# Kernel tuning notes

Hardware: AMD Instinct MI355X
Metric: run time of the kernel (lower is better)

The kernel has to match this reference:

```python
import jax, jax.numpy as jnp
import numpy as np
from jax import lax

SIG_DEPTH = 2
BN_EPS = 1e-5


def zhang_sig(x, depth):
    """Zhang 2D signature of an image batch.

    x: (B, C, H, W). Level-1 term is the total double increment per channel;
    level-(k+1) is built recursively: S_{k+1}[.., c] (i,j) = strict-2D-prefix-sum
    of S_k at (i,j) times the double increment D[c](i,j). Each level k yields
    C^k features (sum over the spatial grid).
    """
    # double (mixed) increments: (B, C, H-1, W-1)
    D = x[:, :, 1:, 1:] - x[:, :, 1:, :-1] - x[:, :, :-1, 1:] + x[:, :, :-1, :-1]
    B, C, h, w = D.shape
    S = D
    levels = [S.sum((-2, -1))]  # (B, C)
    for _ in range(depth - 1):
        # strict 2D prefix sum: P[i,j] = sum_{i'<i, j'<j} S[i',j']
        P = jnp.cumsum(jnp.cumsum(S, axis=-2), axis=-1)
        P = jnp.pad(P, ((0, 0), (0, 0), (1, 0), (1, 0)))[:, :, :-1, :-1]
        # tensor-product with a fresh increment channel: (B, C_prev*C, h, w)
        S = (P[:, :, None] * D[:, None, :]).reshape(B, -1, h, w)
        levels.append(S.sum((-2, -1)))
    return jnp.concatenate(levels, axis=1)  # (B, sum_k C^k)


def setup_inputs() -> dict:
    key = jax.random.key(0)
    ks = jax.random.split(key, 4)
    N, C_IN, C_SIG, HW, NUM_CLASSES = 2048, 64, 32, 8, 100
    F = C_SIG + C_SIG * C_SIG  # 1056 signature features (depth 2)
    feats = jax.random.normal(ks[0], (N, C_IN, HW, HW), dtype=jnp.float32)
    conv_w = jax.random.normal(ks[1], (C_SIG, C_IN, 3, 3), dtype=jnp.float32) * (1.0 / np.sqrt(C_IN * 9))
    bn_gamma = jnp.ones((F,), dtype=jnp.float32)
    bn_beta = jnp.zeros((F,), dtype=jnp.float32)
    lin_w = jax.random.normal(ks[2], (F, F), dtype=jnp.float32) * (1.0 / np.sqrt(F))
    lin_b = jnp.zeros((F,), dtype=jnp.float32)
    fc_w = jax.random.normal(ks[3], (NUM_CLASSES, F), dtype=jnp.float32) * (1.0 / np.sqrt(F))
    fc_b = jnp.zeros((NUM_CLASSES,), dtype=jnp.float32)
    return {"feats": feats, "conv_w": conv_w, "bn_gamma": bn_gamma, "bn_beta": bn_beta,
            "lin_w": lin_w, "lin_b": lin_b, "fc_w": fc_w, "fc_b": fc_b}


def reference(feats, conv_w, bn_gamma, bn_beta, lin_w, lin_b, fc_w, fc_b):
    # Conv2d(64->32, 3x3, stride 1, pad 1, no bias)
    y = lax.conv_general_dilated(
        feats, conv_w, window_strides=(1, 1), padding=((1, 1), (1, 1)),
        dimension_numbers=("NCHW", "OIHW", "NCHW"))
    # Zhang 2D signature pooling -> (N, 1056)
    sig = zhang_sig(y, SIG_DEPTH)
    # BatchNorm1d (training mode: batch statistics, biased variance)
    mean = sig.mean(axis=0)
    var = sig.var(axis=0)
    xn = (sig - mean) * lax.rsqrt(var + BN_EPS)
    h = xn * bn_gamma + bn_beta
    # Linear(F -> F) then classifier Linear(F -> num_classes)
    h = h @ lin_w.T + lin_b
    out = h @ fc_w.T + fc_b
    return out
```

## Files before the change

### kernel.cpp

```cpp
#include <hip/hip_runtime.h>

#define N_B   2048
#define F_SIG 1056
#define F_PAD 1088
#define K_CLS 100
#define K_PAD 128
#define KW_PAD 112
#define DROW   52
#define OSPLIT  8
#define OCHUNK 132
#define XW     72
#define SY     32
#define WF_BLKS 280
#define BF0_BLKS 128

typedef __attribute__((ext_vector_type(8))) short s8v;
typedef __attribute__((ext_vector_type(4))) float f4v;

__device__ __host__ __forceinline__ void split_bf16(float x, unsigned& h, unsigned& l) {
    unsigned u = __builtin_bit_cast(unsigned, x);
    unsigned hb = (u + 0x7FFFu + ((u >> 16) & 1u)) >> 16;
    float hf = __builtin_bit_cast(float, hb << 16);
    float r = x - hf;
    unsigned ur = __builtin_bit_cast(unsigned, r);
    unsigned lb = (ur + 0x7FFFu + ((ur >> 16) & 1u)) >> 16;
    h = hb & 0xFFFFu; l = lb & 0xFFFFu;
}

__global__ void k_wt(const float* __restrict__ cw, unsigned short* __restrict__ Ahi,
                     unsigned short* __restrict__ Alo) {
    int t = blockIdx.x * 256 + threadIdx.x;
    if (t >= 36 * 512) return;
    int f = t >> 9, r = t & 511, lane = r >> 3, e = r & 7;
    int mt = f & 1, ch = (f >> 1) & 1, tap = f >> 2;
    int oc  = mt * 16 + (lane & 15);
    int cin = ch * 32 + (lane >> 4) * 8 + e;
    float v = cw[oc * 576 + cin * 9 + tap];
    unsigned h, l;
    split_bf16(v, h, l);
    Ahi[t] = (unsigned short)h;
    Alo[t] = (unsigned short)l;
}

#define WF_FMA16(sv, vv) do { \
    A0.x = fmaf((sv).x, (vv).x, A0.x); A0.y = fmaf((sv).x, (vv).y, A0.y); \
    A0.z = fmaf((sv).x, (vv).z, A0.z); A0.w = fmaf((sv).x, (vv).w, A0.w); \
    A1.x = fmaf((sv).y, (vv).x, A1.x); A1.y = fmaf((sv).y, (vv).y, A1.y); \
    A1.z = fmaf((sv).y, (vv).z, A1.z); A1.w = fmaf((sv).y, (vv).w, A1.w); \
    A2.x = fmaf((sv).z, (vv).x, A2.x); A2.y = fmaf((sv).z, (vv).y, A2.y); \
    A2.z = fmaf((sv).z, (vv).z, A2.z); A2.w = fmaf((sv).z, (vv).w, A2.w); \
    A3.x = fmaf((sv).w, (vv).x, A3.x); A3.y = fmaf((sv).w, (vv).y, A3.y); \
    A3.z = fmaf((sv).w, (vv).z, A3.z); A3.w = fmaf((sv).w, (vv).w, A3.w); } while (0)

__launch_bounds__(256, 5)
__global__ void k_fused(const float* __restrict__ x,
                        const unsigned short* __restrict__ Ahi,
                        const unsigned short* __restrict__ Alo,
                        float* __restrict__ sig,
                        const float* __restrict__ fcw, const float* __restrict__ lw,
                        float* __restrict__ part,
                        const float* __restrict__ linb, const float* __restrict__ fcb,
                        float* __restrict__ bfv) {
    __shared__ __align__(16) unsigned short xpl[2][100 * XW];
    unsigned short* xhi = xpl[0];
    unsigned short* xlo = xpl[1];
    const int tid = threadIdx.x;
    const int bid = blockIdx.x;

    if (bid < WF_BLKS) {
        const int ibx = bid % 5, ky = (bid / 5) % 7, z = bid / 35;
        const int wv = tid >> 6;
        const int k0 = ky * 16 + wv * 4;
        const int ib = ibx * 256 + (tid & 63) * 4;
        if (ib >= F_SIG) return;
        const float* f0 = fcw + (size_t)min(k0,     K_CLS - 1) * F_SIG;
        const float* f1 = fcw + (size_t)min(k0 + 1, K_CLS - 1) * F_SIG;
        const float* f2 = fcw + (size_t)min(k0 + 2, K_CLS - 1) * F_SIG;
        const float* f3 = fcw + (size_t)min(k0 + 3, K_CLS - 1) * F_SIG;
        const int o0 = z * OCHUNK;
        float4 A0 = {0.f,0.f,0.f,0.f}, A1 = {0.f,0.f,0.f,0.f};
        float4 A2 = {0.f,0.f,0.f,0.f}, A3 = {0.f,0.f,0.f,0.f};
        const float* lwb = lw + (size_t)o0 * F_SIG + ib;
        for (int g = 0; g < OCHUNK / 4; ++g) {
            const int o = o0 + g * 4;
            float4 s0 = *reinterpret_cast<const float4*>(f0 + o);
            float4 s1 = *reinterpret_cast<const float4*>(f1 + o);
            float4 s2 = *reinterpret_cast<const float4*>(f2 + o);
            float4 s3 = *reinterpret_cast<const float4*>(f3 + o);
            const float* lp = lwb + (size_t)(g * 4) * F_SIG;
            float4 v0 = *reinterpret_cast<const float4*>(lp);
            float4 v1 = *reinterpret_cast<const float4*>(lp + F_SIG);
            float4 v2 = *reinterpret_cast<const float4*>(lp + 2 * F_SIG);
            float4 v3 = *reinterpret_cast<const float4*>(lp + 3 * F_SIG);
            float4 sj0 = make_float4(s0.x, s1.x, s2.x, s3.x);
            float4 sj1 = make_float4(s0.y, s1.y, s2.y, s3.y);
            float4 sj2 = make_float4(s0.z, s1.z, s2.z, s3.z);
            float4 sj3 = make_float4(s0.w, s1.w, s2.w, s3.w);
            WF_FMA16(sj0, v0);
            WF_FMA16(sj1, v1);
            WF_FMA16(sj2, v2);
            WF_FMA16(sj3, v3);
        }
        *reinterpret_cast<float4*>(part + ((size_t)z * KW_PAD + k0 + 0) * F_SIG + ib) = A0;
        *reinterpret_cast<float4*>(part + ((size_t)z * KW_PAD + k0 + 1) * F_SIG + ib) = A1;
        *reinterpret_cast<float4*>(part + ((size_t)z * KW_PAD + k0 + 2) * F_SIG + ib) = A2;
        *reinterpret_cast<float4*>(part + ((size_t)z * KW_PAD + k0 + 3) * F_SIG + ib) = A3;
        return;
    }
    if (bid < WF_BLKS + BF0_BLKS) {
        const int k = bid - WF_BLKS;
        float s = 0.f;
        if (k < K_CLS) {
            const float* fr = fcw + (size_t)k * F_SIG;
            for (int o = tid; o < F_SIG; o += 256) s = fmaf(fr[o], linb[o], s);
        }
#pragma unroll
        for (int d = 32; d; d >>= 1) s += __shfl_xor(s, d);
        float* redf = (float*)xhi;
        if ((tid & 63) == 0) redf[tid >> 6] = s;
        __syncthreads();
        if (tid == 0) {
            float tot = redf[0] + redf[1] + redf[2] + redf[3];
            bfv[k] = (k < K_CLS) ? (tot + fcb[k]) : 0.f;
        }
        return;
    }

    const int b = bid - (WF_BLKS + BF0_BLKS);
    float* ysT  = (float*)xpl;
    float* Ds   = ysT + 2304;
    float* Cs   = Ds + 1664;
    float* colS = Cs + 1664;

    for (int e = tid; e < 1296; e += 256) {
        int bb = e / 36, w = e - bb * 36;
        int pp = (bb < 10) ? bb
               : (bb < 20) ? 90 + (bb - 10)
               : ((bb - 20) >> 1) * 10 + 10 + (((bb - 20) & 1) ? 9 : 0);
        reinterpret_cast<unsigned*>(xhi + pp * XW)[w] = 0u;
        reinterpret_cast<unsigned*>(xlo + pp * XW)[w] = 0u;
    }
    const float4* xb4 = reinterpret_cast<const float4*>(x + (size_t)b * 4096);
    {
        float4 v0 = xb4[tid], v1 = xb4[tid + 256], v2 = xb4[tid + 512], v3 = xb4[tid + 768];
#pragma unroll
        for (int u = 0; u < 4; ++u) {
            float4 v = (u == 0) ? v0 : (u == 1) ? v1 : (u == 2) ? v2 : v3;
            int e = tid + u * 256;
            int cin = e >> 4, p = (e & 15) * 4;
            int ih = p >> 3, iw = p & 7;
            int pp = (ih + 1) * 10 + (iw + 1);
            unsigned h, l;
            split_bf16(v.x, h, l); xhi[(pp+0)*XW + cin] = (unsigned short)h; xlo[(pp+0)*XW + cin] = (unsigned short)l;
            split_bf16(v.y, h, l); xhi[(pp+1)*XW + cin] = (unsigned short)h; xlo[(pp+1)*XW + cin] = (unsigned short)l;
            split_bf16(v.z, h, l); xhi[(pp+2)*XW + cin] = (unsigned short)h; xlo[(pp+2)*XW + cin] = (unsigned short)l;
            split_bf16(v.w, h, l); xhi[(pp+3)*XW + cin] = (unsigned short)h; xlo[(pp+3)*XW + cin] = (unsigned short)l;
        }
    }
    __syncthreads();

    f4v accA = {0.f, 0.f, 0.f, 0.f};
    f4v accB = {0.f, 0.f, 0.f, 0.f};
    int pa_, pb_, mt_, kg_;
    {
        const int wv = tid >> 6;
        const int lane = tid & 63;
        const int j16 = lane & 15, kg = lane >> 4;
        const int mt = wv & 1, pt = wv >> 1;
        const int pa = pt * 32 + j16;
        const int pb = pt * 32 + 16 + j16;
        pa_ = pa; pb_ = pb; mt_ = mt; kg_ = kg;
        const int oha = pa >> 3, owa = pa & 7;
        const int ohb = pb >> 3, owb = pb & 7;
        const unsigned short* HbA = xhi + (oha * 10 + owa) * XW + kg * 8;
        const unsigned short* LbA = xlo + (oha * 10 + owa) * XW + kg * 8;
        const unsigned short* HbB = xhi + (ohb * 10 + owb) * XW + kg * 8;
        const unsigned short* LbB = xlo + (ohb * 10 + owb) * XW + kg * 8;
        const uint4* AH = reinterpret_cast<const uint4*>(Ahi) + (size_t)mt * 64 + lane;
        const uint4* AL = reinterpret_cast<const uint4*>(Alo) + (size_t)mt * 64 + lane;
#pragma unroll
        for (int k = 0; k < 18; ++k) {
            const int tap = k >> 1, ch = k & 1;
            const int th = tap / 3, tw = tap % 3;
            const int xoff = (th * 10 + tw) * XW + ch * 32;
            uint4 ah = AH[(size_t)(2 * k) * 64];
            uint4 al = AL[(size_t)(2 * k) * 64];
            uint4 bha = *reinterpret_cast<const uint4*>(HbA + xoff);
            uint4 bla = *reinterpret_cast<const uint4*>(LbA + xoff);
            uint4 bhb = *reinterpret_cast<const uint4*>(HbB + xoff);
            uint4 blb = *reinterpret_cast<const uint4*>(LbB + xoff);
            s8v Ah = __builtin_bit_cast(s8v, ah);
            s8v Al = __builtin_bit_cast(s8v, al);
            s8v BhA = __builtin_bit_cast(s8v, bha);
            s8v BlA = __builtin_bit_cast(s8v, bla);
            s8v BhB = __builtin_bit_cast(s8v, bhb);
            s8v BlB = __builtin_bit_cast(s8v, blb);
            accA = __builtin_amdgcn_mfma_f32_16x16x32_bf16(Ah, BhA, accA, 0, 0, 0);
            accA = __builtin_amdgcn_mfma_f32_16x16x32_bf16(Ah, BlA, accA, 0, 0, 0);
            accA = __builtin_amdgcn_mfma_f32_16x16x32_bf16(Al, BhA, accA, 0, 0, 0);
            accB = __builtin_amdgcn_mfma_f32_16x16x32_bf16(Ah, BhB, accB, 0, 0, 0);
            accB = __builtin_amdgcn_mfma_f32_16x16x32_bf16(Ah, BlB, accB, 0, 0, 0);
            accB = __builtin_amdgcn_mfma_f32_16x16x32_bf16(Al, BhB, accB, 0, 0, 0);
        }
    }
    __syncthreads();
    *reinterpret_cast<f4v*>(ysT + pa_ * 36 + mt_ * 16 + kg_ * 4) = accA;
    *reinterpret_cast<f4v*>(ysT + pb_ * 36 + mt_ * 16 + kg_ * 4) = accB;
    __syncthreads();

    if (tid < 224) {
        const int c = tid / 7, j = tid - (tid / 7) * 7;
        float a  = ysT[j * 36 + c];
        float bq = ysT[(j + 1) * 36 + c];
        float run = 0.f;
        float* Dc = Ds + c * DROW;
        float* Cc = Cs + c * DROW;
#pragma unroll
        for (int i = 0; i < 7; ++i) {
            float a2 = ysT[((i + 1) * 8 + j) * 36 + c];
            float b2 = ysT[((i + 1) * 8 + j + 1) * 36 + c];
            float d = (b2 - a2) - (bq - a);
            Dc[i * 7 + j] = d;
            Cc[i * 7 + j] = run;
            run += d;
            a = a2; bq = b2;
        }
        colS[c * 8 + j] = run;
    } else {
        const int c = tid - 224;
        Ds[c * DROW + 49] = 0.f; Ds[c * DROW + 50] = 0.f; Ds[c * DROW + 51] = 0.f;
    }
    __syncthreads();

    if (tid < 224) {
        const int c = tid / 7, i = tid - (tid / 7) * 7;
        float* Cc = Cs + c * DROW + i * 7;
        float run = 0.f;
#pragma unroll
        for (int j = 0; j < 7; ++j) {
            float v = Cc[j];
            Cc[j] = run;
            run += v;
        }
    } else {
        const int c = tid - 224;
        Cs[c * DROW + 49] = 0.f; Cs[c * DROW + 50] = 0.f; Cs[c * DROW + 51] = 0.f;
    }
    __syncthreads();

    {
        const int bc1 = tid >> 4, bc2 = tid & 15;
        const float* P0 = Cs + bc1 * DROW;
        const float* P1 = Cs + (bc1 + 16) * DROW;
        const float* D0 = Ds + bc2 * DROW;
        const float* D1 = Ds + (bc2 + 16) * DROW;
        float a00 = 0.f, a01 = 0.f, a10 = 0.f, a11 = 0.f;
#pragma unroll
        for (int qb = 0; qb < DROW; qb += 4) {
            float4 p0 = *reinterpret_cast<const float4*>(P0 + qb);
            float4 p1 = *reinterpret_cast<const float4*>(P1 + qb);
            float4 d0 = *reinterpret_cast<const float4*>(D0 + qb);
            float4 d1 = *reinterpret_cast<const float4*>(D1 + qb);
            a00 += p0.x*d0.x + p0.y*d0.y + p0.z*d0.z + p0.w*d0.w;
            a01 += p0.x*d1.x + p0.y*d1.y + p0.z*d1.z + p0.w*d1.w;
            a10 += p1.x*d0.x + p1.y*d0.y + p1.z*d0.z + p1.w*d0.w;
            a11 += p1.x*d1.x + p1.y*d1.y + p1.z*d1.z + p1.w*d1.w;
        }
        float* so = sig + (size_t)b * F_PAD + 32;
        so[bc1 * 32 + bc2]               = a00;
        so[bc1 * 32 + (bc2 + 16)]        = a01;
        so[(bc1 + 16) * 32 + bc2]        = a10;
        so[(bc1 + 16) * 32 + (bc2 + 16)] = a11;
    }

    if (tid < 32) {
        const float* cr = colS + tid * 8;
        float s = cr[0] + cr[1] + cr[2] + cr[3] + cr[4] + cr[5] + cr[6];
        sig[(size_t)b * F_PAD + tid] = s;
    } else if (tid < 64) {
        sig[(size_t)b * F_PAD + F_SIG + (tid - 32)] = 0.f;
    }
}

__global__ void k_stats(const float* __restrict__ sig, float* __restrict__ psum,
                        float* __restrict__ psq) {
    int f = blockIdx.x * 256 + threadIdx.x;
    if (f >= F_SIG) return;
    int y = blockIdx.y;
    const float* sp = sig + (size_t)(y * 64) * F_PAD + f;
    float s = 0.f, q = 0.f;
    for (int r = 0; r < 64; r += 4) {
        float v0 = sp[(size_t)(r + 0) * F_PAD];
        float v1 = sp[(size_t)(r + 1) * F_PAD];
        float v2 = sp[(size_t)(r + 2) * F_PAD];
        float v3 = sp[(size_t)(r + 3) * F_PAD];
        s += v0 + v1 + v2 + v3;
        q = fmaf(v0, v0, q); q = fmaf(v1, v1, q);
        q = fmaf(v2, v2, q); q = fmaf(v3, v3, q);
    }
    psum[(size_t)y * F_PAD + f] = s;
    psq[(size_t)y * F_PAD + f]  = q;
}

__launch_bounds__(64)
__global__ void k_wfred(const float* __restrict__ part,
                        const float* __restrict__ psum, const float* __restrict__ psq,
                        const float* __restrict__ gamma, const float* __restrict__ beta,
                        float* __restrict__ WfT, float* __restrict__ bfv) {
    const int i = blockIdx.x * 64 + threadIdx.x;
    const int k = blockIdx.y;
    float a = 0.f, bb = 0.f;
    if (i < F_SIG) {
        float s = 0.f, q = 0.f;
#pragma unroll
        for (int z = 0; z < SY; ++z) {
            s += psum[(size_t)z * F_PAD + i];
            q += psq[(size_t)z * F_PAD + i];
        }
        float m   = s * (1.f / 2048.f);
        float var = q * (1.f / 2048.f) - m * m;
        a  = gamma[i] / sqrtf(var + 1e-5f);
        bb = beta[i] - m * a;
    }
    const bool valid = (i < F_SIG) && (k < K_CLS);
    float s = 0.f;
    if (valid) {
#pragma unroll
        for (int z = 0; z < OSPLIT; ++z)
            s += part[((size_t)z * KW_PAD + k) * F_SIG + i];
    }
    if (i < F_SIG)
        WfT[(size_t)i * K_PAD + k] = valid ? a * s : 0.f;
    float pb = valid ? bb * s : 0.f;
#pragma unroll
    for (int d = 32; d; d >>= 1) pb += __shfl_xor(pb, d);
    if (threadIdx.x == 0 && k < K_CLS) atomicAdd(&bfv[k], pb);
}

__launch_bounds__(256, 4)
__global__ void k_out3(const float* __restrict__ sig, const float* __restrict__ WfT,
                       const float* __restrict__ bf, float* __restrict__ out) {
    __shared__ __align__(16) float slT[F_SIG * 8];
    const int tid = threadIdx.x;
    const int r0 = blockIdx.x * 8;
    for (int e = tid; e < 8 * (F_SIG / 4); e += 256) {
        int row = e & 7, c4 = e >> 3;
        float4 v = *reinterpret_cast<const float4*>(sig + (size_t)(r0 + row) * F_PAD + c4 * 4);
        slT[(c4 * 4 + 0) * 8 + row] = v.x;
        slT[(c4 * 4 + 1) * 8 + row] = v.y;
        slT[(c4 * 4 + 2) * 8 + row] = v.z;
        slT[(c4 * 4 + 3) * 8 + row] = v.w;
    }
    __syncthreads();

    const int wv = tid >> 6, lane = tid & 63;
    const int i0 = wv * 264;
    const float2* Wp = reinterpret_cast<const float2*>(WfT) + lane;
    float2 acc[8];
#pragma unroll
    for (int r = 0; r < 8; ++r) acc[r] = make_float2(0.f, 0.f);
    for (int g = 0; g < 33; ++g) {
        const int ib = i0 + g * 8;
        float2 w0 = Wp[(size_t)(ib + 0) * 64];
        float2 w1 = Wp[(size_t)(ib + 1) * 64];
        float2 w2 = Wp[(size_t)(ib + 2) * 64];
        float2 w3 = Wp[(size_t)(ib + 3) * 64];
        float2 w4 = Wp[(size_t)(ib + 4) * 64];
        float2 w5 = Wp[(size_t)(ib + 5) * 64];
        float2 w6 = Wp[(size_t)(ib + 6) * 64];
        float2 w7 = Wp[(size_t)(ib + 7) * 64];
#pragma unroll
        for (int j = 0; j < 8; ++j) {
            float2 wj = (j == 0) ? w0 : (j == 1) ? w1 : (j == 2) ? w2 : (j == 3) ? w3
                      : (j == 4) ? w4 : (j == 5) ? w5 : (j == 6) ? w6 : w7;
            const float4* sp = reinterpret_cast<const float4*>(slT + (ib + j) * 8);
            float4 ra = sp[0], rb = sp[1];
            acc[0].x = fmaf(ra.x, wj.x, acc[0].x); acc[0].y = fmaf(ra.x, wj.y, acc[0].y);
            acc[1].x = fmaf(ra.y, wj.x, acc[1].x); acc[1].y = fmaf(ra.y, wj.y, acc[1].y);
            acc[2].x = fmaf(ra.z, wj.x, acc[2].x); acc[2].y = fmaf(ra.z, wj.y, acc[2].y);
            acc[3].x = fmaf(ra.w, wj.x, acc[3].x); acc[3].y = fmaf(ra.w, wj.y, acc[3].y);
            acc[4].x = fmaf(rb.x, wj.x, acc[4].x); acc[4].y = fmaf(rb.x, wj.y, acc[4].y);
            acc[5].x = fmaf(rb.y, wj.x, acc[5].x); acc[5].y = fmaf(rb.y, wj.y, acc[5].y);
            acc[6].x = fmaf(rb.z, wj.x, acc[6].x); acc[6].y = fmaf(rb.z, wj.y, acc[6].y);
            acc[7].x = fmaf(rb.w, wj.x, acc[7].x); acc[7].y = fmaf(rb.w, wj.y, acc[7].y);
        }
    }
    __syncthreads();
    float* red = slT;
    float2* rp = reinterpret_cast<float2*>(red) + wv * 512 + lane;
#pragma unroll
    for (int r = 0; r < 8; ++r) rp[r * 64] = acc[r];
    __syncthreads();
#pragma unroll
    for (int j = 0; j < 4; ++j) {
        int idx = j * 256 + tid;
        int r = idx >> 7, k = idx & 127;
        float s = red[idx] + red[idx + 1024] + red[idx + 2048] + red[idx + 3072];
        if (k < K_CLS) out[(size_t)(r0 + r) * K_CLS + k] = s + bf[k];
    }
}

extern "C" void kernel_launch(void* const* d_in, const int* in_sizes, int n_in,
                              void* d_out, int out_size, void* d_ws, size_t ws_size,
                              hipStream_t stream) {
    (void)in_sizes; (void)n_in; (void)out_size; (void)ws_size;
    const float* feats = (const float*)d_in[0];
    const float* convw = (const float*)d_in[1];
    const float* gamma = (const float*)d_in[2];
    const float* beta  = (const float*)d_in[3];
    const float* linw  = (const float*)d_in[4];
    const float* linb  = (const float*)d_in[5];
    const float* fcw   = (const float*)d_in[6];
    const float* fcb   = (const float*)d_in[7];
    float* out = (float*)d_out;

    float* ws   = (float*)d_ws;
    float* sig  = ws;
    float* psum = sig + (size_t)N_B * F_PAD;
    float* psq  = psum + (size_t)SY * F_PAD;
    float* part = psq + (size_t)SY * F_PAD;
    float* WfT  = part + (size_t)OSPLIT * KW_PAD * F_SIG;
    float* bfv  = WfT + (size_t)F_SIG * K_PAD;
    unsigned short* Ahi = (unsigned short*)(bfv + K_PAD);
    unsigned short* Alo = Ahi + 36 * 512;

    k_wt<<<72, 256, 0, stream>>>(convw, Ahi, Alo);
    k_fused<<<WF_BLKS + BF0_BLKS + N_B, 256, 0, stream>>>(feats, Ahi, Alo, sig,
                                                          fcw, linw, part, linb, fcb, bfv);
    k_stats<<<dim3(5, SY), 256, 0, stream>>>(sig, psum, psq);
    k_wfred<<<dim3(17, K_PAD), 64, 0, stream>>>(part, psum, psq, gamma, beta, WfT, bfv);
    k_out3<<<N_B / 8, 256, 0, stream>>>(sig, WfT, bfv, out);
}
```

Baseline: 74.14 us.

## Split conv MFMA over input-channel halves, reusing B fragments across output tiles

Reorganizes the conv MFMA work so each wave covers both 16-row output-channel tiles for half of the input channels, instead of one output tile across all input channels. Each B (activation) fragment loaded from LDS now feeds two accumulators, which halves LDS reads of the split-bf16 activations per MFMA. The cost is four accumulators per lane instead of two and an extra reduction pass through shared memory with an additional barrier to sum the two channel halves.

```diff
diff --git a/kernel.cpp b/kernel.cpp
--- a/kernel.cpp
+++ b/kernel.cpp
@@ -159,53 +159,76 @@
     }
     __syncthreads();
 
-    f4v accA = {0.f, 0.f, 0.f, 0.f};
-    f4v accB = {0.f, 0.f, 0.f, 0.f};
-    int pa_, pb_, mt_, kg_;
+    f4v a00 = {0.f,0.f,0.f,0.f};
+    f4v a01 = {0.f,0.f,0.f,0.f};
+    f4v b00 = {0.f,0.f,0.f,0.f};
+    f4v b01 = {0.f,0.f,0.f,0.f};
+    int pa_, pb_, kg_, chh_;
     {
         const int wv = tid >> 6;
         const int lane = tid & 63;
         const int j16 = lane & 15, kg = lane >> 4;
-        const int mt = wv & 1, pt = wv >> 1;
+        const int pt = wv >> 1, chh = wv & 1;
         const int pa = pt * 32 + j16;
-        const int pb = pt * 32 + 16 + j16;
-        pa_ = pa; pb_ = pb; mt_ = mt; kg_ = kg;
+        const int pb = pa + 16;
+        pa_ = pa; pb_ = pb; kg_ = kg; chh_ = chh;
         const int oha = pa >> 3, owa = pa & 7;
         const int ohb = pb >> 3, owb = pb & 7;
-        const unsigned short* HbA = xhi + (oha * 10 + owa) * XW + kg * 8;
-        const unsigned short* LbA = xlo + (oha * 10 + owa) * XW + kg * 8;
-        const unsigned short* HbB = xhi + (ohb * 10 + owb) * XW + kg * 8;
-        const unsigned short* LbB = xlo + (ohb * 10 + owb) * XW + kg * 8;
-        const uint4* AH = reinterpret_cast<const uint4*>(Ahi) + (size_t)mt * 64 + lane;
-        const uint4* AL = reinterpret_cast<const uint4*>(Alo) + (size_t)mt * 64 + lane;
-#pragma unroll
-        for (int k = 0; k < 18; ++k) {
-            const int tap = k >> 1, ch = k & 1;
+        const unsigned short* HbA = xhi + (oha * 10 + owa) * XW + chh * 32 + kg * 8;
+        const unsigned short* LbA = xlo + (oha * 10 + owa) * XW + chh * 32 + kg * 8;
+        const unsigned short* HbB = xhi + (ohb * 10 + owb) * XW + chh * 32 + kg * 8;
+        const unsigned short* LbB = xlo + (ohb * 10 + owb) * XW + chh * 32 + kg * 8;
+        const uint4* AH = reinterpret_cast<const uint4*>(Ahi) + (size_t)chh * 128 + lane;
+        const uint4* AL = reinterpret_cast<const uint4*>(Alo) + (size_t)chh * 128 + lane;
+#pragma unroll
+        for (int tap = 0; tap < 9; ++tap) {
             const int th = tap / 3, tw = tap % 3;
-            const int xoff = (th * 10 + tw) * XW + ch * 32;
-            uint4 ah = AH[(size_t)(2 * k) * 64];
-            uint4 al = AL[(size_t)(2 * k) * 64];
+            const int xoff = (th * 10 + tw) * XW;
+            uint4 h0 = AH[(size_t)(tap * 4) * 64];
+            uint4 l0 = AL[(size_t)(tap * 4) * 64];
+            uint4 h1 = AH[(size_t)(tap * 4 + 1) * 64];
+            uint4 l1 = AL[(size_t)(tap * 4 + 1) * 64];
             uint4 bha = *reinterpret_cast<const uint4*>(HbA + xoff);
             uint4 bla = *reinterpret_cast<const uint4*>(LbA + xoff);
             uint4 bhb = *reinterpret_cast<const uint4*>(HbB + xoff);
             uint4 blb = *reinterpret_cast<const uint4*>(LbB + xoff);
-            s8v Ah = __builtin_bit_cast(s8v, ah);
-            s8v Al = __builtin_bit_cast(s8v, al);
+            s8v A0h = __builtin_bit_cast(s8v, h0);
+            s8v A0l = __builtin_bit_cast(s8v, l0);
+            s8v A1h = __builtin_bit_cast(s8v, h1);
+            s8v A1l = __builtin_bit_cast(s8v, l1);
             s8v BhA = __builtin_bit_cast(s8v, bha);
             s8v BlA = __builtin_bit_cast(s8v, bla);
             s8v BhB = __builtin_bit_cast(s8v, bhb);
             s8v BlB = __builtin_bit_cast(s8v, blb);
-            accA = __builtin_amdgcn_mfma_f32_16x16x32_bf16(Ah, BhA, accA, 0, 0, 0);
-            accA = __builtin_amdgcn_mfma_f32_16x16x32_bf16(Ah, BlA, accA, 0, 0, 0);
-            accA = __builtin_amdgcn_mfma_f32_16x16x32_bf16(Al, BhA, accA, 0, 0, 0);
-            accB = __builtin_amdgcn_mfma_f32_16x16x32_bf16(Ah, BhB, accB, 0, 0, 0);
-            accB = __builtin_amdgcn_mfma_f32_16x16x32_bf16(Ah, BlB, accB, 0, 0, 0);
-            accB = __builtin_amdgcn_mfma_f32_16x16x32_bf16(Al, BhB, accB, 0, 0, 0);
-        }
-    }
-    __syncthreads();
-    *reinterpret_cast<f4v*>(ysT + pa_ * 36 + mt_ * 16 + kg_ * 4) = accA;
-    *reinterpret_cast<f4v*>(ysT + pb_ * 36 + mt_ * 16 + kg_ * 4) = accB;
+            a00 = __builtin_amdgcn_mfma_f32_16x16x32_bf16(A0h, BhA, a00, 0, 0, 0);
+            a00 = __builtin_amdgcn_mfma_f32_16x16x32_bf16(A0h, BlA, a00, 0, 0, 0);
+            a00 = __builtin_amdgcn_mfma_f32_16x16x32_bf16(A0l, BhA, a00, 0, 0, 0);
+            a01 = __builtin_amdgcn_mfma_f32_16x16x32_bf16(A1h, BhA, a01, 0, 0, 0);
+            a01 = __builtin_amdgcn_mfma_f32_16x16x32_bf16(A1h, BlA, a01, 0, 0, 0);
+            a01 = __builtin_amdgcn_mfma_f32_16x16x32_bf16(A1l, BhA, a01, 0, 0, 0);
+            b00 = __builtin_amdgcn_mfma_f32_16x16x32_bf16(A0h, BhB, b00, 0, 0, 0);
+            b00 = __builtin_amdgcn_mfma_f32_16x16x32_bf16(A0h, BlB, b00, 0, 0, 0);
+            b00 = __builtin_amdgcn_mfma_f32_16x16x32_bf16(A0l, BhB, b00, 0, 0, 0);
+            b01 = __builtin_amdgcn_mfma_f32_16x16x32_bf16(A1h, BhB, b01, 0, 0, 0);
+            b01 = __builtin_amdgcn_mfma_f32_16x16x32_bf16(A1h, BlB, b01, 0, 0, 0);
+            b01 = __builtin_amdgcn_mfma_f32_16x16x32_bf16(A1l, BhB, b01, 0, 0, 0);
+        }
+    }
+    __syncthreads();
+    if (chh_ == 0) {
+        *reinterpret_cast<f4v*>(ysT + pa_ * 36 + kg_ * 4)      = a00;
+        *reinterpret_cast<f4v*>(ysT + pa_ * 36 + 16 + kg_ * 4) = a01;
+        *reinterpret_cast<f4v*>(ysT + pb_ * 36 + kg_ * 4)      = b00;
+        *reinterpret_cast<f4v*>(ysT + pb_ * 36 + 16 + kg_ * 4) = b01;
+    }
+    __syncthreads();
+    if (chh_ == 1) {
+        f4v* p0 = reinterpret_cast<f4v*>(ysT + pa_ * 36 + kg_ * 4);
+        f4v* p1 = reinterpret_cast<f4v*>(ysT + pa_ * 36 + 16 + kg_ * 4);
+        f4v* p2 = reinterpret_cast<f4v*>(ysT + pb_ * 36 + kg_ * 4);
+        f4v* p3 = reinterpret_cast<f4v*>(ysT + pb_ * 36 + 16 + kg_ * 4);
+        *p0 += a00; *p1 += a01; *p2 += b00; *p3 += b01;
+    }
     __syncthreads();
 
     if (tid < 224) {
@@ -254,23 +277,23 @@
         const float* P1 = Cs + (bc1 + 16) * DROW;
         const float* D0 = Ds + bc2 * DROW;
         const float* D1 = Ds + (bc2 + 16) * DROW;
-        float a00 = 0.f, a01 = 0.f, a10 = 0.f, a11 = 0.f;
+        float a00v = 0.f, a01v = 0.f, a10v = 0.f, a11v = 0.f;
 #pragma unroll
         for (int qb = 0; qb < DROW; qb += 4) {
             float4 p0 = *reinterpret_cast<const float4*>(P0 + qb);
             float4 p1 = *reinterpret_cast<const float4*>(P1 + qb);
             float4 d0 = *reinterpret_cast<const float4*>(D0 + qb);
             float4 d1 = *reinterpret_cast<const float4*>(D1 + qb);
-            a00 += p0.x*d0.x + p0.y*d0.y + p0.z*d0.z + p0.w*d0.w;
-            a01 += p0.x*d1.x + p0.y*d1.y + p0.z*d1.z + p0.w*d1.w;
-            a10 += p1.x*d0.x + p1.y*d0.y + p1.z*d0.z + p1.w*d0.w;
-            a11 += p1.x*d1.x + p1.y*d1.y + p1.z*d1.z + p1.w*d1.w;
+            a00v += p0.x*d0.x + p0.y*d0.y + p0.z*d0.z + p0.w*d0.w;
+            a01v += p0.x*d1.x + p0.y*d1.y + p0.z*d1.z + p0.w*d1.w;
+            a10v += p1.x*d0.x + p1.y*d0.y + p1.z*d0.z + p1.w*d0.w;
+            a11v += p1.x*d1.x + p1.y*d1.y + p1.z*d1.z + p1.w*d1.w;
         }
         float* so = sig + (size_t)b * F_PAD + 32;
-        so[bc1 * 32 + bc2]               = a00;
-        so[bc1 * 32 + (bc2 + 16)]        = a01;
-        so[(bc1 + 16) * 32 + bc2]        = a10;
-        so[(bc1 + 16) * 32 + (bc2 + 16)] = a11;
+        so[bc1 * 32 + bc2]               = a00v;
+        so[bc1 * 32 + (bc2 + 16)]        = a01v;
+        so[(bc1 + 16) * 32 + bc2]        = a10v;
+        so[(bc1 + 16) * 32 + (bc2 + 16)] = a11v;
     }
 
     if (tid < 32) {
```

After: 71.60 us. -3.4%, faster.
